# Performance work log

Hardware: AMD Instinct MI355X
Metric: run time of the kernel (lower is better)

The kernel has to match this reference:

```python
import jax, jax.numpy as jnp
import numpy as np

B, I, H = 16384, 1024, 1024
W_SCALE = 0.03  # keep gate pre-activations in a sane range (mimics small init)


def setup_inputs() -> dict:
    key = jax.random.key(0)
    ks = jax.random.split(key, 7)
    return {
        "x": jax.random.normal(ks[0], (B, I), dtype=jnp.float32),
        "c": jax.random.normal(ks[1], (B, H), dtype=jnp.float32),
        "h": jax.random.normal(ks[2], (B, H), dtype=jnp.float32),
        # gate order along axis 0: f (forget), i (input), k (cell cand), o (output)
        "Wx": jax.random.normal(ks[3], (4, H, I), dtype=jnp.float32) * W_SCALE,
        "bx": jax.random.normal(ks[4], (4, H), dtype=jnp.float32) * W_SCALE,
        "Wh": jax.random.normal(ks[5], (4, H, H), dtype=jnp.float32) * W_SCALE,
        "bh": jax.random.normal(ks[6], (4, H), dtype=jnp.float32) * W_SCALE,
    }


def reference(x, c, h, Wx, bx, Wh, bh):
    # Fused equivalent of the 8 tiny nn.Linear calls: one stacked GEMM each
    # for input->hidden and hidden->hidden. pre: [B, 4, H]
    pre = (jnp.einsum('bi,ghi->bgh', x, Wx)
           + jnp.einsum('bk,ghk->bgh', h, Wh)
           + bx[None] + bh[None])
    f = jax.nn.sigmoid(pre[:, 0])   # forget gate (w1/r1)
    i = jax.nn.sigmoid(pre[:, 1])   # input gate  (w2/r2)
    k = jnp.tanh(pre[:, 2])         # cell candidate (w3/r3)
    o = jax.nn.sigmoid(pre[:, 3])   # output gate (w4/r4)
    c_new = f * c + i * k
    h_new = o * jnp.tanh(c_new)
    return (o, c_new, h_new)
```

## Files before the change

kernel.cpp:

```cpp
#include <hip/hip_runtime.h>
#include <hip/hip_bf16.h>
#include <cstdint>

#define DI __device__ __forceinline__

typedef __attribute__((ext_vector_type(4))) float f32x4;
typedef __attribute__((ext_vector_type(8))) short bf16x8;

static constexpr int B_ = 16384, I_ = 1024, H_ = 1024;
static constexpr int M = B_;
static constexpr int N = 4 * H_;
static constexpr int K = I_ + H_;
static constexpr int NT = K / 64;

static constexpr size_t OFF_A  = 0;
static constexpr size_t OFF_W  = OFF_A + (size_t)M * K * 2;
static constexpr size_t OFF_BI = OFF_W + (size_t)N * K * 2;

DI unsigned short f2bf(float f) {
    union { float f; unsigned u; } v; v.f = f;
    unsigned r = v.u + 0x7FFFu + ((v.u >> 16) & 1u);
    return (unsigned short)(r >> 16);
}

__global__ void cvt_a(const float* __restrict__ x, const float* __restrict__ h,
                      unsigned short* __restrict__ A)
{
    long tid = (long)blockIdx.x * blockDim.x + threadIdx.x;
    long row = tid >> 9;
    int  col = (int)(tid & 511) * 4;
    const float* src = (col < I_) ? x + (size_t)row * I_ + col
                                  : h + (size_t)row * H_ + (col - I_);
    float4 v = *(const float4*)src;
    ushort4 o;
    o.x = f2bf(v.x); o.y = f2bf(v.y); o.z = f2bf(v.z); o.w = f2bf(v.w);
    *(ushort4*)(A + (size_t)row * K + col) = o;
}

__global__ void cvt_w2(const float* __restrict__ Wx, const float* __restrict__ Wh,
                       unsigned short* __restrict__ W2)
{
    int tid  = blockIdx.x * blockDim.x + threadIdx.x;
    int lane = tid & 63;
    int s    = (tid >> 6) & 63;
    int f    = tid >> 12;
    int col16 = lane & 15;
    int gate  = f & 3;
    int hcol  = ((f >> 2) << 4) | col16;
    int srow  = gate * H_ + hcol;
    int k0    = (s << 5) + ((lane >> 4) << 3);

    const float* p = (k0 < I_) ? Wx + (size_t)srow * I_ + k0
                               : Wh + (size_t)srow * H_ + (k0 - I_);
    float4 v0 = *(const float4*)p;
    float4 v1 = *(const float4*)(p + 4);
    unsigned short o[8] = { f2bf(v0.x), f2bf(v0.y), f2bf(v0.z), f2bf(v0.w),
                            f2bf(v1.x), f2bf(v1.y), f2bf(v1.z), f2bf(v1.w) };
    *(ushort4*)(W2 + (((size_t)f * 64 + s) << 9) + (lane << 3))     = *(ushort4*)&o[0];
    *(ushort4*)(W2 + (((size_t)f * 64 + s) << 9) + (lane << 3) + 4) = *(ushort4*)&o[4];
}

__global__ void bias_kernel(const float* __restrict__ bx, const float* __restrict__ bh,
                            float* __restrict__ bias)
{
    int r = blockIdx.x * blockDim.x + threadIdx.x;
    if (r < N) {
        int gate = (r >> 4) & 3;
        int hcol = ((r >> 6) << 4) | (r & 15);
        int s = gate * H_ + hcol;
        bias[r] = bx[s] + bh[s];
    }
}

DI void stage_half(const unsigned short* __restrict__ g, int grow0, int kcol,
                   unsigned short* ldsbase, int tid)
{
    const int w    = tid >> 6, lane = tid & 63;
    const int rsub = (w << 3) + (lane >> 3);
    const int kk   = kcol + (((lane & 7) ^ (lane >> 3)) << 3);
#pragma unroll
    for (int l = 0; l < 2; ++l) {
        const unsigned short* gp = g + (size_t)(grow0 + (l << 6) + rsub) * K + kk;
        unsigned short* lp = ldsbase + (((l << 6) + (w << 3)) << 6);
        __builtin_amdgcn_global_load_lds(
            (const __attribute__((address_space(1))) void*)gp,
            (__attribute__((address_space(3))) void*)lp, 16, 0, 0);
    }
}

DI bf16x8 ldfrag(const unsigned short* tile, int row, int ks, int lane)
{
    const int sl = ((ks << 2) + (lane >> 4)) ^ (lane & 7);
    return *(const bf16x8*)(tile + (row << 6) + (sl << 3));
}

DI float sigf(float v) { return 1.f / (1.f + __expf(-v)); }
DI float tanhfast(float v) {
    float vc = fminf(fmaxf(v, -15.f), 15.f);
    float e  = __expf(2.f * vc);
    return (e - 1.f) / (e + 1.f);
}

__global__ __launch_bounds__(512, 2) void gemm_lstm(
    const unsigned short* __restrict__ Abf, const unsigned short* __restrict__ W2,
    const float* __restrict__ bias, const float* __restrict__ c,
    float* __restrict__ out)
{
    __shared__ __align__(16) unsigned short sh[32768];

    const int tid  = threadIdx.x;
    const int lane = tid & 63;
    const int wid  = tid >> 6;
    const int wr   = wid >> 2;
    const int wc   = wid & 3;

    const int bid  = blockIdx.x;
    const int xcd  = bid & 7;
    const int loc  = bid >> 3;
    const int nbk  = (xcd << 1) | (loc & 1);
    const int mbk  = loc >> 1;
    const int brow = mbk << 8, bcol = nbk << 8;

    const int l15  = lane & 15;
    const int rA0  = (wr << 7) + l15;
    const int nf0  = (bcol >> 4) + (wc << 2);

    const unsigned short* w2p = W2 + (lane << 3);

    f32x4 acc[8][4];
#pragma unroll
    for (int i = 0; i < 8; ++i)
#pragma unroll
        for (int j = 0; j < 4; ++j) acc[i][j] = f32x4{0.f, 0.f, 0.f, 0.f};
    bf16x8 a[4][2], b[4][2];

    {
        stage_half(Abf, brow,       0, sh,        tid);
        stage_half(Abf, brow + 128, 0, sh + 8192, tid);
        asm volatile("s_waitcnt vmcnt(0)" ::: "memory");
        __builtin_amdgcn_s_barrier();
    }

    for (int t = 0; t < NT; ++t) {
        const int q = t & 1;
        unsigned short* curA = sh + (q << 14);
        unsigned short* nxtA = sh + ((q ^ 1) << 14);
        const int k1 = ((t + 1) & 31) << 6;

        stage_half(Abf, brow,       k1, nxtA,        tid);
        stage_half(Abf, brow + 128, k1, nxtA + 8192, tid);

#pragma unroll
        for (int n = 0; n < 4; ++n)
#pragma unroll
            for (int ks = 0; ks < 2; ++ks)
                b[n][ks] = *(const bf16x8*)(
                    w2p + (((size_t)(nf0 + n) * 64 + (t << 1) + ks) << 9));

#pragma unroll
        for (int m = 0; m < 4; ++m)
#pragma unroll
            for (int ks = 0; ks < 2; ++ks)
                a[m][ks] = ldfrag(curA, rA0 + m * 16, ks, lane);

#pragma unroll
        for (int ks = 0; ks < 2; ++ks)
#pragma unroll
            for (int m = 0; m < 4; ++m)
#pragma unroll
                for (int n = 0; n < 4; ++n)
                    acc[m][n] = __builtin_amdgcn_mfma_f32_16x16x32_bf16(
                        a[m][ks], b[n][ks], acc[m][n], 0, 0, 0);

#pragma unroll
        for (int m = 0; m < 4; ++m)
#pragma unroll
            for (int ks = 0; ks < 2; ++ks)
                a[m][ks] = ldfrag(curA, rA0 + 64 + m * 16, ks, lane);

#pragma unroll
        for (int ks = 0; ks < 2; ++ks)
#pragma unroll
            for (int m = 0; m < 4; ++m)
#pragma unroll
                for (int n = 0; n < 4; ++n)
                    acc[4 + m][n] = __builtin_amdgcn_mfma_f32_16x16x32_bf16(
                        a[m][ks], b[n][ks], acc[4 + m][n], 0, 0, 0);

        asm volatile("s_waitcnt vmcnt(0)" ::: "memory");
        __builtin_amdgcn_s_barrier();
    }

    const int hcol  = (((nbk << 2) + wc) << 4) + l15;
    const int crow0 = brow + (wr << 7) + ((lane >> 4) << 2);
    const int cb0   = bcol + (wc << 6) + l15;
    const float bs0 = bias[cb0];
    const float bs1 = bias[cb0 + 16];
    const float bs2 = bias[cb0 + 32];
    const float bs3 = bias[cb0 + 48];
    const size_t P  = (size_t)B_ * H_;
#pragma unroll
    for (int mf = 0; mf < 8; ++mf) {
#pragma unroll
        for (int j = 0; j < 4; ++j) {
            const int row = crow0 + mf * 16 + j;
            const size_t base = (size_t)row * H_ + hcol;
            float fg = sigf(acc[mf][0][j] + bs0);
            float ig = sigf(acc[mf][1][j] + bs1);
            float kg = tanhfast(acc[mf][2][j] + bs2);
            float og = sigf(acc[mf][3][j] + bs3);
            float cv = c[base];
            float cn = fg * cv + ig * kg;
            float hn = og * tanhfast(cn);
            out[base]         = og;
            out[P + base]     = cn;
            out[2 * P + base] = hn;
        }
    }
}

extern "C" void kernel_launch(void* const* d_in, const int* in_sizes, int n_in,
                              void* d_out, int out_size, void* d_ws, size_t ws_size,
                              hipStream_t stream)
{
    const float* x  = (const float*)d_in[0];
    const float* c  = (const float*)d_in[1];
    const float* h  = (const float*)d_in[2];
    const float* Wx = (const float*)d_in[3];
    const float* bx = (const float*)d_in[4];
    const float* Wh = (const float*)d_in[5];
    const float* bh = (const float*)d_in[6];

    unsigned short* Abf  = (unsigned short*)((char*)d_ws + OFF_A);
    unsigned short* W2   = (unsigned short*)((char*)d_ws + OFF_W);
    float*          bias = (float*)((char*)d_ws + OFF_BI);
    float*          out  = (float*)d_out;

    cvt_a<<<(M * 512) / 256, 256, 0, stream>>>(x, h, Abf);
    cvt_w2<<<4096, 256, 0, stream>>>(Wx, Wh, W2);
    bias_kernel<<<16, 256, 0, stream>>>(bx, bh, bias);
    gemm_lstm<<<(M / 256) * (N / 256), 512, 0, stream>>>(
        Abf, W2, bias, c, out);
}
```

Before: 330.6 us.

## Pre-swizzle A into MFMA fragment layout and load directly from global

```diff
diff --git a/kernel.cpp b/kernel.cpp
--- a/kernel.cpp
+++ b/kernel.cpp
@@ -23,18 +23,25 @@
     return (unsigned short)(r >> 16);
 }
 
-__global__ void cvt_a(const float* __restrict__ x, const float* __restrict__ h,
-                      unsigned short* __restrict__ A)
-{
-    long tid = (long)blockIdx.x * blockDim.x + threadIdx.x;
-    long row = tid >> 9;
-    int  col = (int)(tid & 511) * 4;
-    const float* src = (col < I_) ? x + (size_t)row * I_ + col
-                                  : h + (size_t)row * H_ + (col - I_);
-    float4 v = *(const float4*)src;
-    ushort4 o;
-    o.x = f2bf(v.x); o.y = f2bf(v.y); o.z = f2bf(v.z); o.w = f2bf(v.w);
-    *(ushort4*)(A + (size_t)row * K + col) = o;
+__global__ void cvt_a2(const float* __restrict__ x, const float* __restrict__ h,
+                       unsigned short* __restrict__ A2)
+{
+    int tid  = blockIdx.x * blockDim.x + threadIdx.x;
+    int lane = tid & 63;
+    int s    = (tid >> 6) & 63;
+    int mf   = tid >> 12;
+    int row  = (mf << 4) | (lane & 15);
+    int k0   = (s << 5) + ((lane >> 4) << 3);
+
+    const float* p = (k0 < I_) ? x + (size_t)row * I_ + k0
+                               : h + (size_t)row * H_ + (k0 - I_);
+    float4 v0 = *(const float4*)p;
+    float4 v1 = *(const float4*)(p + 4);
+    unsigned short o[8] = { f2bf(v0.x), f2bf(v0.y), f2bf(v0.z), f2bf(v0.w),
+                            f2bf(v1.x), f2bf(v1.y), f2bf(v1.z), f2bf(v1.w) };
+    unsigned short* d = A2 + (((size_t)mf * 64 + s) << 9) + (lane << 3);
+    *(ushort4*)d       = *(ushort4*)&o[0];
+    *(ushort4*)(d + 4) = *(ushort4*)&o[4];
 }
 
 __global__ void cvt_w2(const float* __restrict__ Wx, const float* __restrict__ Wh,
@@ -56,8 +63,9 @@
     float4 v1 = *(const float4*)(p + 4);
     unsigned short o[8] = { f2bf(v0.x), f2bf(v0.y), f2bf(v0.z), f2bf(v0.w),
                             f2bf(v1.x), f2bf(v1.y), f2bf(v1.z), f2bf(v1.w) };
-    *(ushort4*)(W2 + (((size_t)f * 64 + s) << 9) + (lane << 3))     = *(ushort4*)&o[0];
-    *(ushort4*)(W2 + (((size_t)f * 64 + s) << 9) + (lane << 3) + 4) = *(ushort4*)&o[4];
+    unsigned short* d = W2 + (((size_t)f * 64 + s) << 9) + (lane << 3);
+    *(ushort4*)d       = *(ushort4*)&o[0];
+    *(ushort4*)(d + 4) = *(ushort4*)&o[4];
 }
 
 __global__ void bias_kernel(const float* __restrict__ bx, const float* __restrict__ bh,
@@ -72,28 +80,6 @@
     }
 }
 
-DI void stage_half(const unsigned short* __restrict__ g, int grow0, int kcol,
-                   unsigned short* ldsbase, int tid)
-{
-    const int w    = tid >> 6, lane = tid & 63;
-    const int rsub = (w << 3) + (lane >> 3);
-    const int kk   = kcol + (((lane & 7) ^ (lane >> 3)) << 3);
-#pragma unroll
-    for (int l = 0; l < 2; ++l) {
-        const unsigned short* gp = g + (size_t)(grow0 + (l << 6) + rsub) * K + kk;
-        unsigned short* lp = ldsbase + (((l << 6) + (w << 3)) << 6);
-        __builtin_amdgcn_global_load_lds(
-            (const __attribute__((address_space(1))) void*)gp,
-            (__attribute__((address_space(3))) void*)lp, 16, 0, 0);
-    }
-}
-
-DI bf16x8 ldfrag(const unsigned short* tile, int row, int ks, int lane)
-{
-    const int sl = ((ks << 2) + (lane >> 4)) ^ (lane & 7);
-    return *(const bf16x8*)(tile + (row << 6) + (sl << 3));
-}
-
 DI float sigf(float v) { return 1.f / (1.f + __expf(-v)); }
 DI float tanhfast(float v) {
     float vc = fminf(fmaxf(v, -15.f), 15.f);
@@ -102,12 +88,10 @@
 }
 
 __global__ __launch_bounds__(512, 2) void gemm_lstm(
-    const unsigned short* __restrict__ Abf, const unsigned short* __restrict__ W2,
+    const unsigned short* __restrict__ A2, const unsigned short* __restrict__ W2,
     const float* __restrict__ bias, const float* __restrict__ c,
     float* __restrict__ out)
 {
-    __shared__ __align__(16) unsigned short sh[32768];
-
     const int tid  = threadIdx.x;
     const int lane = tid & 63;
     const int wid  = tid >> 6;
@@ -122,9 +106,10 @@
     const int brow = mbk << 8, bcol = nbk << 8;
 
     const int l15  = lane & 15;
-    const int rA0  = (wr << 7) + l15;
+    const int mf0  = (brow >> 4) + (wr << 3);
     const int nf0  = (bcol >> 4) + (wc << 2);
 
+    const unsigned short* a2p = A2 + (lane << 3);
     const unsigned short* w2p = W2 + (lane << 3);
 
     f32x4 acc[8][4];
@@ -134,34 +119,22 @@
         for (int j = 0; j < 4; ++j) acc[i][j] = f32x4{0.f, 0.f, 0.f, 0.f};
     bf16x8 a[4][2], b[4][2];
 
-    {
-        stage_half(Abf, brow,       0, sh,        tid);
-        stage_half(Abf, brow + 128, 0, sh + 8192, tid);
-        asm volatile("s_waitcnt vmcnt(0)" ::: "memory");
-        __builtin_amdgcn_s_barrier();
-    }
-
     for (int t = 0; t < NT; ++t) {
-        const int q = t & 1;
-        unsigned short* curA = sh + (q << 14);
-        unsigned short* nxtA = sh + ((q ^ 1) << 14);
-        const int k1 = ((t + 1) & 31) << 6;
-
-        stage_half(Abf, brow,       k1, nxtA,        tid);
-        stage_half(Abf, brow + 128, k1, nxtA + 8192, tid);
+        const int s2 = t << 1;
 
 #pragma unroll
         for (int n = 0; n < 4; ++n)
 #pragma unroll
             for (int ks = 0; ks < 2; ++ks)
                 b[n][ks] = *(const bf16x8*)(
-                    w2p + (((size_t)(nf0 + n) * 64 + (t << 1) + ks) << 9));
+                    w2p + (((size_t)(nf0 + n) * 64 + s2 + ks) << 9));
 
 #pragma unroll
         for (int m = 0; m < 4; ++m)
 #pragma unroll
             for (int ks = 0; ks < 2; ++ks)
-                a[m][ks] = ldfrag(curA, rA0 + m * 16, ks, lane);
+                a[m][ks] = *(const bf16x8*)(
+                    a2p + (((size_t)(mf0 + m) * 64 + s2 + ks) << 9));
 
 #pragma unroll
         for (int ks = 0; ks < 2; ++ks)
@@ -176,7 +149,8 @@
         for (int m = 0; m < 4; ++m)
 #pragma unroll
             for (int ks = 0; ks < 2; ++ks)
-                a[m][ks] = ldfrag(curA, rA0 + 64 + m * 16, ks, lane);
+                a[m][ks] = *(const bf16x8*)(
+                    a2p + (((size_t)(mf0 + 4 + m) * 64 + s2 + ks) << 9));
 
 #pragma unroll
         for (int ks = 0; ks < 2; ++ks)
@@ -186,9 +160,6 @@
                 for (int n = 0; n < 4; ++n)
                     acc[4 + m][n] = __builtin_amdgcn_mfma_f32_16x16x32_bf16(
                         a[m][ks], b[n][ks], acc[4 + m][n], 0, 0, 0);
-
-        asm volatile("s_waitcnt vmcnt(0)" ::: "memory");
-        __builtin_amdgcn_s_barrier();
     }
 
     const int hcol  = (((nbk << 2) + wc) << 4) + l15;
@@ -231,14 +202,14 @@
     const float* Wh = (const float*)d_in[5];
     const float* bh = (const float*)d_in[6];
 
-    unsigned short* Abf  = (unsigned short*)((char*)d_ws + OFF_A);
+    unsigned short* A2   = (unsigned short*)((char*)d_ws + OFF_A);
     unsigned short* W2   = (unsigned short*)((char*)d_ws + OFF_W);
     float*          bias = (float*)((char*)d_ws + OFF_BI);
     float*          out  = (float*)d_out;
 
-    cvt_a<<<(M * 512) / 256, 256, 0, stream>>>(x, h, Abf);
+    cvt_a2<<<16384, 256, 0, stream>>>(x, h, A2);
     cvt_w2<<<4096, 256, 0, stream>>>(Wx, Wh, W2);
     bias_kernel<<<16, 256, 0, stream>>>(bx, bh, bias);
     gemm_lstm<<<(M / 256) * (N / 256), 512, 0, stream>>>(
-        Abf, W2, bias, c, out);
-}
+        A2, W2, bias, c, out);
+}
```

After: 430.8 us. +30.3%, slower.
